# Performance work log

Measured on AMD Instinct MI355X. Metric: run time of the kernel, lower is better.

The kernel has to match this reference:

```python
import jax, jax.numpy as jnp
import numpy as np

VOCAB_SIZE = 13
EMBED_DIM = 50
HIDDEN_DIM = 50
BATCH = 2048
SEQ_LEN = 2048


def setup_inputs() -> dict:
    key = jax.random.key(0)
    ks = jax.random.split(key, 10)
    s = 0.1
    return {
        "x": jax.random.randint(ks[0], (BATCH, SEQ_LEN), 0, VOCAB_SIZE),
        "embed": jax.random.normal(ks[1], (VOCAB_SIZE, EMBED_DIM), jnp.float32),
        "W_ih": jax.random.normal(ks[2], (4 * HIDDEN_DIM, EMBED_DIM), jnp.float32) * s,
        "W_hh": jax.random.normal(ks[3], (4 * HIDDEN_DIM, HIDDEN_DIM), jnp.float32) * s,
        "b_ih": jax.random.normal(ks[4], (4 * HIDDEN_DIM,), jnp.float32) * s,
        "b_hh": jax.random.normal(ks[5], (4 * HIDDEN_DIM,), jnp.float32) * s,
        "W1": jax.random.normal(ks[6], (HIDDEN_DIM, HIDDEN_DIM), jnp.float32) * s,
        "b1": jax.random.normal(ks[7], (HIDDEN_DIM,), jnp.float32) * s,
        "W2": jax.random.normal(ks[8], (1, HIDDEN_DIM), jnp.float32) * s,
        "b2": jax.random.normal(ks[9], (1,), jnp.float32) * s,
    }


def reference(x, embed, W_ih, W_hh, b_ih, b_hh, W1, b1, W2, b2):
    B = x.shape[0]
    H = HIDDEN_DIM
    embeds = embed[x]                    # [B, T, E]
    xs = jnp.swapaxes(embeds, 0, 1)      # [T, B, E] for scan over time

    def step(carry, xt):
        hx, cx = carry
        gates = xt @ W_ih.T + b_ih + hx @ W_hh.T + b_hh   # [B, 4H]
        i = jax.nn.sigmoid(gates[:, 0 * H:1 * H])
        f = jax.nn.sigmoid(gates[:, 1 * H:2 * H])
        g = jnp.tanh(gates[:, 2 * H:3 * H])
        o = jax.nn.sigmoid(gates[:, 3 * H:4 * H])
        cx = f * cx + i * g
        hx = o * jnp.tanh(cx)
        return (hx, cx), None

    init = (jnp.zeros((B, H), embeds.dtype), jnp.zeros((B, H), embeds.dtype))
    (hx, _), _ = jax.lax.scan(step, init, xs)

    h = jax.nn.relu(hx @ W1.T + b1)
    out = (h @ W2.T + b2).squeeze(1)     # [B]
    return out
```

## Files before the change

### kernel.cpp

```cpp
#include <hip/hip_runtime.h>
#include <hip/hip_fp16.h>

#define T_SEQ 2048
#define HID   50
#define KP    64
#define MB    4
#define NBLK  512
#define NTHR  256
#define HSTR  80
#define BUFB  (MB*HSTR)

#define NLOG2E  1.4426950408889634f
#define N2LOG2E 2.8853900817779268f

typedef __attribute__((ext_vector_type(8))) _Float16 half8;
typedef __attribute__((ext_vector_type(4))) float    f32x4;

__device__ __forceinline__ ushort f16b(float f){ return __half_as_ushort(__float2half(f)); }
__device__ __forceinline__ float rcp_(float x){ return __builtin_amdgcn_rcpf(x); }
__device__ __forceinline__ float ex2_(float x){ return __builtin_amdgcn_exp2f(x); }

__global__ void build_B(const float* __restrict__ embed, const float* __restrict__ Wih,
                        const float* __restrict__ Whh, const float* __restrict__ bih,
                        const float* __restrict__ bhh, ushort* __restrict__ Bm) {
    int idx = blockIdx.x * blockDim.x + threadIdx.x;
    if (idx >= 256 * KP) return;
    int col = idx >> 6, k = idx & 63;
    int wq = col >> 6, g = (col >> 4) & 3, cc = col & 15;
    int u = wq * 16 + cc;
    ushort v = 0;
    if (u < HID) {
        int r = g * HID + u;
        float s = (g == 2) ? -N2LOG2E : -NLOG2E;
        if (k < HID) {
            v = f16b(s * Whh[r * HID + k]);
        } else if (k < 63) {
            float t = 0.f;
            for (int e = 0; e < HID; ++e)
                t = fmaf(embed[(k - 50) * HID + e], Wih[r * HID + e], t);
            v = f16b(s * t);
        } else {
            v = f16b(s * (bih[r] + bhh[r]));
        }
    }
    Bm[idx] = v;
}

__global__ __launch_bounds__(NTHR, 2) void lstm4(
    const int*    __restrict__ x,
    const ushort* __restrict__ Bm,
    const float*  __restrict__ W1,
    const float*  __restrict__ b1,
    const float*  __restrict__ W2,
    const float*  __restrict__ b2,
    float*        __restrict__ out)
{
    const int t   = threadIdx.x;
    const int w   = t >> 6;
    const int l   = t & 63;
    const int q   = l >> 4;
    const int c16 = l & 15;
    const int u   = w * 16 + c16;
    const int wu  = __builtin_amdgcn_readfirstlane(w);

    __shared__ __align__(16) ushort hbuf[2 * BUFB];
    __shared__ float zb[HID * MB];

    half8 bf[4][2];
    {
        const ushort* bp = Bm + (w * 64 + c16) * KP + q * 8;
        #pragma unroll
        for (int j = 0; j < 4; ++j) {
            bf[j][0] = *(const half8*)(bp + j * 16 * KP);
            bf[j][1] = *(const half8*)(bp + j * 16 * KP + 32);
        }
    }
    #pragma unroll
    for (int j = 0; j < 4; ++j)
        asm volatile("" : "+v"(bf[j][0]), "+v"(bf[j][1]));

    for (int i = t; i < 2 * BUFB; i += NTHR) hbuf[i] = 0;

    const int  row0 = blockIdx.x * MB;
    const int* xrow = x + (long)row0 * T_SEQ + (long)wu * T_SEQ;
    __syncthreads();
    int tk0 = xrow[0];
    int tk1 = xrow[1];
    if (l == 0) {
        hbuf[0 * BUFB + wu * HSTR + 63] = 0x3C00;
        hbuf[1 * BUFB + wu * HSTR + 63] = 0x3C00;
        hbuf[0 * BUFB + wu * HSTR + 50 + tk0] = 0x3C00;
        hbuf[1 * BUFB + wu * HSTR + 50 + tk1] = 0x3C00;
    }
    int t0r = tk1, t1r = tk0, t2r = tk1;
    __syncthreads();

    {
        uint slot = __builtin_amdgcn_s_getreg(6148) & 0xF;
        if (slot & 1) __builtin_amdgcn_s_sleep(6);
    }

    const ushort* ar  = hbuf + (c16 >> 2) * HSTR + q * 8;
    ushort*       wr_ = hbuf + q * HSTR + u;
    ushort*       hbw = hbuf + wu * HSTR + 50;

    float cs = 0.f;

#define STEP(P) do {                                                              \
        int it = step + 2 + (P); if (it > T_SEQ - 1) it = T_SEQ - 1;              \
        int tknf = xrow[it];                     \
        half8 a0 = *(const half8*)(ar + (P) * BUFB);                              \
        half8 a1 = *(const half8*)(ar + (P) * BUFB + 32);                         \
        const f32x4 zz = {0.f, 0.f, 0.f, 0.f};                                    \
        __builtin_amdgcn_s_setprio(1);                                            \
        f32x4 z0 = __builtin_amdgcn_mfma_f32_16x16x32_f16(a0, bf[0][0], zz,0,0,0);\
        z0 = __builtin_amdgcn_mfma_f32_16x16x32_f16(a1, bf[0][1], z0, 0,0,0);     \
        f32x4 z1 = __builtin_amdgcn_mfma_f32_16x16x32_f16(a0, bf[1][0], zz,0,0,0);\
        z1 = __builtin_amdgcn_mfma_f32_16x16x32_f16(a1, bf[1][1], z1, 0,0,0);     \
        f32x4 z2 = __builtin_amdgcn_mfma_f32_16x16x32_f16(a0, bf[2][0], zz,0,0,0);\
        z2 = __builtin_amdgcn_mfma_f32_16x16x32_f16(a1, bf[2][1], z2, 0,0,0);     \
        f32x4 z3 = __builtin_amdgcn_mfma_f32_16x16x32_f16(a0, bf[3][0], zz,0,0,0);\
        z3 = __builtin_amdgcn_mfma_f32_16x16x32_f16(a1, bf[3][1], z3, 0,0,0);     \
        __builtin_amdgcn_s_setprio(0);                                            \
           \
        float pi = ex2_(fminf(z0[0], 30.f));                          \
        float pf = ex2_(fminf(z1[0], 30.f));                          \
        float qg = ex2_(fminf(z2[0], 30.f));                          \
        float Df = 1.f + pf;                                                      \
        float D2 = (1.f + pi) * (1.f + qg);                                       \
        float iv1 = rcp_(Df * D2);                                                \
        float fv  = iv1 * D2;                                       \
        float igs = iv1 * Df * fmaf(N2LOG2E, qg, -N2LOG2E);      \
        cs = fmaf(fv, cs, igs);                                                   \
        float po = ex2_(fminf(z3[0], 30.f));                          \
        float qc = ex2_(fminf(cs, 30.f));                       \
        float iv2 = rcp_((1.f + po) * (1.f + qc));                                \
        float hh  = iv2 * (1.f - qc);                       \
        if (u < HID) wr_[(1 - (P)) * BUFB] = f16b(hh);                            \
        if (l == 0) {                                                             \
            ushort* hb = hbw + (1 - (P)) * BUFB;                                  \
            hb[t0r] = 0;                                                          \
            hb[t2r] = 0x3C00;                                                     \
        }                                                                         \
        t0r = t1r; t1r = t2r; t2r = tknf;                                         \
        __syncthreads();                                                          \
    } while (0)

    #pragma unroll 1
    for (int step = 0; step < T_SEQ; step += 2) {
        STEP(0);
        STEP(1);
    }
#undef STEP

    if (t < MB * HID) {
        int m = t & 3, uu = t >> 2;
        float a = b1[uu];
        const ushort* hr = hbuf + m * HSTR;
        #pragma unroll 10
        for (int k = 0; k < HID; ++k)
            a = fmaf(W1[uu * HID + k], __half2float(__ushort_as_half(hr[k])), a);
        zb[uu * MB + m] = fmaxf(a, 0.f);
    }
    __syncthreads();
    if (t < MB) {
        float a = b2[0];
        #pragma unroll 10
        for (int j = 0; j < HID; ++j)
            a = fmaf(W2[j], zb[j * MB + t], a);
        out[row0 + t] = a;
    }
}

extern "C" void kernel_launch(void* const* d_in, const int* in_sizes, int n_in,
                              void* d_out, int out_size, void* d_ws, size_t ws_size,
                              hipStream_t stream) {
    const int*   x     = (const int*)  d_in[0];
    const float* embed = (const float*)d_in[1];
    const float* W_ih  = (const float*)d_in[2];
    const float* W_hh  = (const float*)d_in[3];
    const float* b_ih  = (const float*)d_in[4];
    const float* b_hh  = (const float*)d_in[5];
    const float* W1    = (const float*)d_in[6];
    const float* b1    = (const float*)d_in[7];
    const float* W2    = (const float*)d_in[8];
    const float* b2    = (const float*)d_in[9];
    float* out = (float*)d_out;

    ushort* Bm = (ushort*)d_ws;

    build_B<<<(256 * KP + NTHR - 1) / NTHR, NTHR, 0, stream>>>(
        embed, W_ih, W_hh, b_ih, b_hh, Bm);

    lstm4<<<NBLK, NTHR, 0, stream>>>(
        x, Bm, W1, b1, W2, b2, out);
}
```

Before: 692.7 us.

## Interleave two independent batch groups per block and stage tokens in LDS

Each block now processes 8 sequences as two independent 4-row groups, issuing both groups' MFMAs and gate math within one step so the two dependency chains can hide each other's latency under a single barrier. The grid is halved to 256 blocks with launch bounds of 1 block per CU. Token indices for the block are preloaded into LDS as bytes, replacing per-step global loads. The per-slot sleep and setprio tricks are removed. In exchange, per-step instruction count doubles and occupancy drops, which can lengthen the serial step if latency was not the bottleneck.

After: 954.0 us. 1.38x slower.

```diff
diff --git a/kernel.cpp b/kernel.cpp
--- a/kernel.cpp
+++ b/kernel.cpp
@@ -4,11 +4,11 @@
 #define T_SEQ 2048
 #define HID   50
 #define KP    64
-#define MB    4
-#define NBLK  512
+#define MBG   4
+#define NBLK  256
 #define NTHR  256
 #define HSTR  80
-#define BUFB  (MB*HSTR)
+#define BUFB  (MBG*HSTR)
 
 #define NLOG2E  1.4426950408889634f
 #define N2LOG2E 2.8853900817779268f
@@ -46,7 +46,7 @@
     Bm[idx] = v;
 }
 
-__global__ __launch_bounds__(NTHR, 2) void lstm4(
+__global__ __launch_bounds__(NTHR, 1) void lstm_dual(
     const int*    __restrict__ x,
     const ushort* __restrict__ Bm,
     const float*  __restrict__ W1,
@@ -61,10 +61,11 @@
     const int q   = l >> 4;
     const int c16 = l & 15;
     const int u   = w * 16 + c16;
-    const int wu  = __builtin_amdgcn_readfirstlane(w);
-
-    __shared__ __align__(16) ushort hbuf[2 * BUFB];
-    __shared__ float zb[HID * MB];
+
+    __shared__ __align__(16) ushort hb0[2 * BUFB];
+    __shared__ __align__(16) ushort hb1[2 * BUFB];
+    __shared__ __align__(16) unsigned char tokL[8 * T_SEQ];
+    __shared__ float zb[HID * 8];
 
     half8 bf[4][2];
     {
@@ -79,70 +80,104 @@
     for (int j = 0; j < 4; ++j)
         asm volatile("" : "+v"(bf[j][0]), "+v"(bf[j][1]));
 
-    for (int i = t; i < 2 * BUFB; i += NTHR) hbuf[i] = 0;
-
-    const int  row0 = blockIdx.x * MB;
-    const int* xrow = x + (long)row0 * T_SEQ + (long)wu * T_SEQ;
+    {
+        const int4* xs = (const int4*)(x + (long)blockIdx.x * 8 * T_SEQ);
+        for (int i = t; i < 8 * T_SEQ / 4; i += NTHR) {
+            int4 v = xs[i];
+            uint pk = (uint)(v.x & 0xFF) | ((uint)(v.y & 0xFF) << 8) |
+                      ((uint)(v.z & 0xFF) << 16) | ((uint)(v.w & 0xFF) << 24);
+            *(uint*)(tokL + i * 4) = pk;
+        }
+    }
+    for (int i = t; i < 2 * BUFB; i += NTHR) { hb0[i] = 0; hb1[i] = 0; }
     __syncthreads();
-    int tk0 = xrow[0];
-    int tk1 = xrow[1];
-    if (l == 0) {
-        hbuf[0 * BUFB + wu * HSTR + 63] = 0x3C00;
-        hbuf[1 * BUFB + wu * HSTR + 63] = 0x3C00;
-        hbuf[0 * BUFB + wu * HSTR + 50 + tk0] = 0x3C00;
-        hbuf[1 * BUFB + wu * HSTR + 50 + tk1] = 0x3C00;
-    }
-    int t0r = tk1, t1r = tk0, t2r = tk1;
+
+    int tA0, tA1, tA2, tB0, tB1, tB2;
+    {
+        int k00 = tokL[w * T_SEQ + 0],       k01 = tokL[w * T_SEQ + 1];
+        int k10 = tokL[(4 + w) * T_SEQ + 0], k11 = tokL[(4 + w) * T_SEQ + 1];
+        if (l == 0) {
+            hb0[0 * BUFB + w * HSTR + 63] = 0x3C00;
+            hb0[1 * BUFB + w * HSTR + 63] = 0x3C00;
+            hb0[0 * BUFB + w * HSTR + 50 + k00] = 0x3C00;
+            hb0[1 * BUFB + w * HSTR + 50 + k01] = 0x3C00;
+            hb1[0 * BUFB + w * HSTR + 63] = 0x3C00;
+            hb1[1 * BUFB + w * HSTR + 63] = 0x3C00;
+            hb1[0 * BUFB + w * HSTR + 50 + k10] = 0x3C00;
+            hb1[1 * BUFB + w * HSTR + 50 + k11] = 0x3C00;
+        }
+        tA0 = k01; tA1 = k00; tA2 = k01;
+        tB0 = k11; tB1 = k10; tB2 = k11;
+    }
     __syncthreads();
 
-    {
-        uint slot = __builtin_amdgcn_s_getreg(6148) & 0xF;
-        if (slot & 1) __builtin_amdgcn_s_sleep(6);
-    }
-
-    const ushort* ar  = hbuf + (c16 >> 2) * HSTR + q * 8;
-    ushort*       wr_ = hbuf + q * HSTR + u;
-    ushort*       hbw = hbuf + wu * HSTR + 50;
-
-    float cs = 0.f;
-
+    const ushort* ar0 = hb0 + (c16 >> 2) * HSTR + q * 8;
+    const ushort* ar1 = hb1 + (c16 >> 2) * HSTR + q * 8;
+    ushort*       wr0 = hb0 + q * HSTR + u;
+    ushort*       wr1 = hb1 + q * HSTR + u;
+    const unsigned char* tp0 = tokL + w * T_SEQ;
+    const unsigned char* tp1 = tokL + (4 + w) * T_SEQ;
+
+    float cs0 = 0.f, cs1 = 0.f;
+
+#define MFMA_(A,B,C) __builtin_amdgcn_mfma_f32_16x16x32_f16((A),(B),(C),0,0,0)
 #define STEP(P) do {                                                              \
         int it = step + 2 + (P); if (it > T_SEQ - 1) it = T_SEQ - 1;              \
-        int tknf = xrow[it];                     \
-        half8 a0 = *(const half8*)(ar + (P) * BUFB);                              \
-        half8 a1 = *(const half8*)(ar + (P) * BUFB + 32);                         \
+        int tn0 = tp0[it];                               \
+        int tn1 = tp1[it];                                                        \
+        half8 a00 = *(const half8*)(ar0 + (P) * BUFB);                            \
+        half8 a01 = *(const half8*)(ar0 + (P) * BUFB + 32);                       \
+        half8 a10 = *(const half8*)(ar1 + (P) * BUFB);                            \
+        half8 a11 = *(const half8*)(ar1 + (P) * BUFB + 32);                       \
         const f32x4 zz = {0.f, 0.f, 0.f, 0.f};                                    \
-        __builtin_amdgcn_s_setprio(1);                                            \
-        f32x4 z0 = __builtin_amdgcn_mfma_f32_16x16x32_f16(a0, bf[0][0], zz,0,0,0);\
-        z0 = __builtin_amdgcn_mfma_f32_16x16x32_f16(a1, bf[0][1], z0, 0,0,0);     \
-        f32x4 z1 = __builtin_amdgcn_mfma_f32_16x16x32_f16(a0, bf[1][0], zz,0,0,0);\
-        z1 = __builtin_amdgcn_mfma_f32_16x16x32_f16(a1, bf[1][1], z1, 0,0,0);     \
-        f32x4 z2 = __builtin_amdgcn_mfma_f32_16x16x32_f16(a0, bf[2][0], zz,0,0,0);\
-        z2 = __builtin_amdgcn_mfma_f32_16x16x32_f16(a1, bf[2][1], z2, 0,0,0);     \
-        f32x4 z3 = __builtin_amdgcn_mfma_f32_16x16x32_f16(a0, bf[3][0], zz,0,0,0);\
-        z3 = __builtin_amdgcn_mfma_f32_16x16x32_f16(a1, bf[3][1], z3, 0,0,0);     \
-        __builtin_amdgcn_s_setprio(0);                                            \
-           \
-        float pi = ex2_(fminf(z0[0], 30.f));                          \
-        float pf = ex2_(fminf(z1[0], 30.f));                          \
-        float qg = ex2_(fminf(z2[0], 30.f));                          \
-        float Df = 1.f + pf;                                                      \
-        float D2 = (1.f + pi) * (1.f + qg);                                       \
-        float iv1 = rcp_(Df * D2);                                                \
-        float fv  = iv1 * D2;                                       \
-        float igs = iv1 * Df * fmaf(N2LOG2E, qg, -N2LOG2E);      \
-        cs = fmaf(fv, cs, igs);                                                   \
-        float po = ex2_(fminf(z3[0], 30.f));                          \
-        float qc = ex2_(fminf(cs, 30.f));                       \
-        float iv2 = rcp_((1.f + po) * (1.f + qc));                                \
-        float hh  = iv2 * (1.f - qc);                       \
-        if (u < HID) wr_[(1 - (P)) * BUFB] = f16b(hh);                            \
+        f32x4 z0 = MFMA_(a00, bf[0][0], zz); z0 = MFMA_(a01, bf[0][1], z0);       \
+        f32x4 z1 = MFMA_(a00, bf[1][0], zz); z1 = MFMA_(a01, bf[1][1], z1);       \
+        f32x4 z2 = MFMA_(a00, bf[2][0], zz); z2 = MFMA_(a01, bf[2][1], z2);       \
+        f32x4 z3 = MFMA_(a00, bf[3][0], zz); z3 = MFMA_(a01, bf[3][1], z3);       \
+        f32x4 y0 = MFMA_(a10, bf[0][0], zz); y0 = MFMA_(a11, bf[0][1], y0);       \
+        f32x4 y1 = MFMA_(a10, bf[1][0], zz); y1 = MFMA_(a11, bf[1][1], y1);       \
+        f32x4 y2 = MFMA_(a10, bf[2][0], zz); y2 = MFMA_(a11, bf[2][1], y2);       \
+        f32x4 y3 = MFMA_(a10, bf[3][0], zz); y3 = MFMA_(a11, bf[3][1], y3);       \
+          \
+        float pi0 = ex2_(fminf(z0[0], 30.f));                                     \
+        float pf0 = ex2_(fminf(z1[0], 30.f));                                     \
+        float qg0 = ex2_(fminf(z2[0], 30.f));                                     \
+        float Df0 = 1.f + pf0;                                                    \
+        float D20 = (1.f + pi0) * (1.f + qg0);                                    \
+        float ivA = rcp_(Df0 * D20);                                              \
+        float fv0 = ivA * D20;                                                    \
+        float ig0 = ivA * Df0 * fmaf(N2LOG2E, qg0, -N2LOG2E);                     \
+        cs0 = fmaf(fv0, cs0, ig0);                                                \
+        float po0 = ex2_(fminf(z3[0], 30.f));                                     \
+        float qc0 = ex2_(fminf(cs0, 30.f));                                       \
+        float ivB = rcp_((1.f + po0) * (1.f + qc0));                              \
+        float h0  = ivB * (1.f - qc0);                                            \
+                   \
+        float pi1 = ex2_(fminf(y0[0], 30.f));                                     \
+        float pf1 = ex2_(fminf(y1[0], 30.f));                                     \
+        float qg1 = ex2_(fminf(y2[0], 30.f));                                     \
+        float Df1 = 1.f + pf1;                                                    \
+        float D21 = (1.f + pi1) * (1.f + qg1);                                    \
+        float ivC = rcp_(Df1 * D21);                                              \
+        float fv1 = ivC * D21;                                                    \
+        float ig1 = ivC * Df1 * fmaf(N2LOG2E, qg1, -N2LOG2E);                     \
+        cs1 = fmaf(fv1, cs1, ig1);                                                \
+        float po1 = ex2_(fminf(y3[0], 30.f));                                     \
+        float qc1 = ex2_(fminf(cs1, 30.f));                                       \
+        float ivD = rcp_((1.f + po1) * (1.f + qc1));                              \
+        float h1  = ivD * (1.f - qc1);                                            \
+        if (u < HID) {                                                            \
+            wr0[(1 - (P)) * BUFB] = f16b(h0);                                     \
+            wr1[(1 - (P)) * BUFB] = f16b(h1);                                     \
+        }                                                                         \
         if (l == 0) {                                                             \
-            ushort* hb = hbw + (1 - (P)) * BUFB;                                  \
-            hb[t0r] = 0;                                                          \
-            hb[t2r] = 0x3C00;                                                     \
+            ushort* p0 = hb0 + (1 - (P)) * BUFB + w * HSTR + 50;                  \
+            p0[tA0] = 0;  p0[tA2] = 0x3C00;                                       \
+            ushort* p1 = hb1 + (1 - (P)) * BUFB + w * HSTR + 50;                  \
+            p1[tB0] = 0;  p1[tB2] = 0x3C00;                                       \
         }                                                                         \
-        t0r = t1r; t1r = t2r; t2r = tknf;                                         \
+        tA0 = tA1; tA1 = tA2; tA2 = tn0;                                          \
+        tB0 = tB1; tB1 = tB2; tB2 = tn1;                                          \
         __syncthreads();                                                          \
     } while (0)
 
@@ -152,23 +187,24 @@
         STEP(1);
     }
 #undef STEP
-
-    if (t < MB * HID) {
-        int m = t & 3, uu = t >> 2;
+#undef MFMA_
+
+    for (int idx = t; idx < 8 * HID; idx += NTHR) {
+        int m = idx & 7, uu = idx >> 3;
+        const ushort* hr = (m < 4 ? hb0 : hb1) + (m & 3) * HSTR;
         float a = b1[uu];
-        const ushort* hr = hbuf + m * HSTR;
         #pragma unroll 10
         for (int k = 0; k < HID; ++k)
             a = fmaf(W1[uu * HID + k], __half2float(__ushort_as_half(hr[k])), a);
-        zb[uu * MB + m] = fmaxf(a, 0.f);
+        zb[uu * 8 + m] = fmaxf(a, 0.f);
     }
     __syncthreads();
-    if (t < MB) {
+    if (t < 8) {
         float a = b2[0];
         #pragma unroll 10
         for (int j = 0; j < HID; ++j)
-            a = fmaf(W2[j], zb[j * MB + t], a);
-        out[row0 + t] = a;
+            a = fmaf(W2[j], zb[j * 8 + t], a);
+        out[blockIdx.x * 8 + t] = a;
     }
 }
 
@@ -192,6 +228,6 @@
     build_B<<<(256 * KP + NTHR - 1) / NTHR, NTHR, 0, stream>>>(
         embed, W_ih, W_hh, b_ih, b_hh, Bm);
 
-    lstm4<<<NBLK, NTHR, 0, stream>>>(
+    lstm_dual<<<NBLK, NTHR, 0, stream>>>(
         x, Bm, W1, b1, W2, b2, out);
 }
```

## Use 8 waves per block handling 8 rows, with DPP gate exchange and LDS tokens

Applied to the files above, without the earlier changes.

Blocks now hold 8 sequences across 8 waves (256 blocks of 512 threads). Each wave covers 8 hidden units using half the MFMAs per step, and the gate columns held in each lane's other half are swapped in with a DPP row-swap. All tokens for the block are preloaded into LDS as bytes, which takes per-step global loads off the serial recurrence path, and the wave-slot sleep staggering is removed. The cost is a 512-thread barrier every step and only 256 blocks, which may leave CUs underused or make synchronisation heavier.

Result: slower. 748.3 us (+8.0%).

```diff
diff --git a/kernel.cpp b/kernel.cpp
--- a/kernel.cpp
+++ b/kernel.cpp
@@ -4,9 +4,9 @@
 #define T_SEQ 2048
 #define HID   50
 #define KP    64
-#define MB    4
-#define NBLK  512
-#define NTHR  256
+#define MB    8
+#define NBLK  256
+#define NTHR  512
 #define HSTR  80
 #define BUFB  (MB*HSTR)
 
@@ -19,6 +19,9 @@
 __device__ __forceinline__ ushort f16b(float f){ return __half_as_ushort(__float2half(f)); }
 __device__ __forceinline__ float rcp_(float x){ return __builtin_amdgcn_rcpf(x); }
 __device__ __forceinline__ float ex2_(float x){ return __builtin_amdgcn_exp2f(x); }
+__device__ __forceinline__ float dpp_swap8(float v){
+    return __int_as_float(__builtin_amdgcn_mov_dpp(__float_as_int(v), 0x128, 0xF, 0xF, true));
+}
 
 __global__ void build_B(const float* __restrict__ embed, const float* __restrict__ Wih,
                         const float* __restrict__ Whh, const float* __restrict__ bih,
@@ -26,8 +29,9 @@
     int idx = blockIdx.x * blockDim.x + threadIdx.x;
     if (idx >= 256 * KP) return;
     int col = idx >> 6, k = idx & 63;
-    int wq = col >> 6, g = (col >> 4) & 3, cc = col & 15;
-    int u = wq * 16 + cc;
+    int w = col >> 5, j = (col >> 4) & 1, cc = col & 15;
+    int g = 2 * j + (cc >> 3);
+    int u = 8 * w + (cc & 7);
     ushort v = 0;
     if (u < HID) {
         int r = g * HID + u;
@@ -46,7 +50,7 @@
     Bm[idx] = v;
 }
 
-__global__ __launch_bounds__(NTHR, 2) void lstm4(
+__global__ __launch_bounds__(NTHR, 2) void lstm8w(
     const int*    __restrict__ x,
     const ushort* __restrict__ Bm,
     const float*  __restrict__ W1,
@@ -55,94 +59,103 @@
     const float*  __restrict__ b2,
     float*        __restrict__ out)
 {
-    const int t   = threadIdx.x;
-    const int w   = t >> 6;
-    const int l   = t & 63;
-    const int q   = l >> 4;
-    const int c16 = l & 15;
-    const int u   = w * 16 + c16;
-    const int wu  = __builtin_amdgcn_readfirstlane(w);
+    const int t    = threadIdx.x;
+    const int w    = t >> 6;
+    const int l    = t & 63;
+    const int q    = l >> 4;
+    const int c16  = l & 15;
+    const bool lo  = (c16 < 8);
+    const int u    = 8 * w + (c16 & 7);
+    const int myrow = 2 * q + (lo ? 0 : 1);
 
     __shared__ __align__(16) ushort hbuf[2 * BUFB];
+    __shared__ __align__(16) unsigned char tokL[MB * T_SEQ];
     __shared__ float zb[HID * MB];
 
-    half8 bf[4][2];
+    half8 bf[2][2];
     {
-        const ushort* bp = Bm + (w * 64 + c16) * KP + q * 8;
+        const ushort* bp = Bm + (w * 32 + c16) * KP + q * 8;
         #pragma unroll
-        for (int j = 0; j < 4; ++j) {
+        for (int j = 0; j < 2; ++j) {
             bf[j][0] = *(const half8*)(bp + j * 16 * KP);
             bf[j][1] = *(const half8*)(bp + j * 16 * KP + 32);
         }
     }
-    #pragma unroll
-    for (int j = 0; j < 4; ++j)
-        asm volatile("" : "+v"(bf[j][0]), "+v"(bf[j][1]));
-
+    asm volatile("" : "+v"(bf[0][0]), "+v"(bf[0][1]), "+v"(bf[1][0]), "+v"(bf[1][1]));
+
+    {
+        const int4* xs = (const int4*)(x + (long)blockIdx.x * MB * T_SEQ);
+        for (int i = t; i < MB * T_SEQ / 4; i += NTHR) {
+            int4 v = xs[i];
+            uint pk = (uint)(v.x & 0xFF) | ((uint)(v.y & 0xFF) << 8) |
+                      ((uint)(v.z & 0xFF) << 16) | ((uint)(v.w & 0xFF) << 24);
+            *(uint*)(tokL + i * 4) = pk;
+        }
+    }
     for (int i = t; i < 2 * BUFB; i += NTHR) hbuf[i] = 0;
-
-    const int  row0 = blockIdx.x * MB;
-    const int* xrow = x + (long)row0 * T_SEQ + (long)wu * T_SEQ;
     __syncthreads();
-    int tk0 = xrow[0];
-    int tk1 = xrow[1];
+
+    int tk0 = tokL[w * T_SEQ + 0];
+    int tk1 = tokL[w * T_SEQ + 1];
     if (l == 0) {
-        hbuf[0 * BUFB + wu * HSTR + 63] = 0x3C00;
-        hbuf[1 * BUFB + wu * HSTR + 63] = 0x3C00;
-        hbuf[0 * BUFB + wu * HSTR + 50 + tk0] = 0x3C00;
-        hbuf[1 * BUFB + wu * HSTR + 50 + tk1] = 0x3C00;
+        hbuf[0 * BUFB + w * HSTR + 63] = 0x3C00;
+        hbuf[1 * BUFB + w * HSTR + 63] = 0x3C00;
+        hbuf[0 * BUFB + w * HSTR + 50 + tk0] = 0x3C00;
+        hbuf[1 * BUFB + w * HSTR + 50 + tk1] = 0x3C00;
     }
     int t0r = tk1, t1r = tk0, t2r = tk1;
     __syncthreads();
 
-    {
-        uint slot = __builtin_amdgcn_s_getreg(6148) & 0xF;
-        if (slot & 1) __builtin_amdgcn_s_sleep(6);
-    }
-
-    const ushort* ar  = hbuf + (c16 >> 2) * HSTR + q * 8;
-    ushort*       wr_ = hbuf + q * HSTR + u;
-    ushort*       hbw = hbuf + wu * HSTR + 50;
+    const ushort* ar  = hbuf + (c16 >> 1) * HSTR + q * 8;
+    ushort*       wr_ = hbuf + myrow * HSTR + u;
+    const unsigned char* tp = tokL + w * T_SEQ;
 
     float cs = 0.f;
 
+#define MFMA_(A,B,C) __builtin_amdgcn_mfma_f32_16x16x32_f16((A),(B),(C),0,0,0)
 #define STEP(P) do {                                                              \
         int it = step + 2 + (P); if (it > T_SEQ - 1) it = T_SEQ - 1;              \
-        int tknf = xrow[it];                     \
+        int tn = tp[it];                                  \
         half8 a0 = *(const half8*)(ar + (P) * BUFB);                              \
         half8 a1 = *(const half8*)(ar + (P) * BUFB + 32);                         \
         const f32x4 zz = {0.f, 0.f, 0.f, 0.f};                                    \
         __builtin_amdgcn_s_setprio(1);                                            \
-        f32x4 z0 = __builtin_amdgcn_mfma_f32_16x16x32_f16(a0, bf[0][0], zz,0,0,0);\
-        z0 = __builtin_amdgcn_mfma_f32_16x16x32_f16(a1, bf[0][1], z0, 0,0,0);     \
-        f32x4 z1 = __builtin_amdgcn_mfma_f32_16x16x32_f16(a0, bf[1][0], zz,0,0,0);\
-        z1 = __builtin_amdgcn_mfma_f32_16x16x32_f16(a1, bf[1][1], z1, 0,0,0);     \
-        f32x4 z2 = __builtin_amdgcn_mfma_f32_16x16x32_f16(a0, bf[2][0], zz,0,0,0);\
-        z2 = __builtin_amdgcn_mfma_f32_16x16x32_f16(a1, bf[2][1], z2, 0,0,0);     \
-        f32x4 z3 = __builtin_amdgcn_mfma_f32_16x16x32_f16(a0, bf[3][0], zz,0,0,0);\
-        z3 = __builtin_amdgcn_mfma_f32_16x16x32_f16(a1, bf[3][1], z3, 0,0,0);     \
+        f32x4 z0a = MFMA_(a0, bf[0][0], zz);    \
+        f32x4 z0b = MFMA_(a1, bf[0][1], zz);                                      \
+        f32x4 z1a = MFMA_(a0, bf[1][0], zz);                                      \
+        f32x4 z1b = MFMA_(a1, bf[1][1], zz);                                      \
         __builtin_amdgcn_s_setprio(0);                                            \
-           \
-        float pi = ex2_(fminf(z0[0], 30.f));                          \
-        float pf = ex2_(fminf(z1[0], 30.f));                          \
-        float qg = ex2_(fminf(z2[0], 30.f));                          \
+        float s0l = z0a[0] + z0b[0];                     \
+        float s0h = z0a[2] + z0b[2];                     \
+        float s1l = z1a[0] + z1b[0];                     \
+        float s1h = z1a[2] + z1b[2];                     \
+        float rx0 = dpp_swap8(lo ? s0h : s0l);    \
+        float rx1 = dpp_swap8(lo ? s1h : s1l);                                    \
+        float gi = lo ? s0l : rx0;                  \
+        float gf = lo ? rx0 : s0h;                                                \
+        float gg = lo ? s1l : rx1;                                                \
+        float go = lo ? rx1 : s1h;                                                \
+                        \
+        float pi = ex2_(fminf(gi, 30.f));                                         \
+        float pf = ex2_(fminf(gf, 30.f));                                         \
+        float qg = ex2_(fminf(gg, 30.f));                                         \
         float Df = 1.f + pf;                                                      \
         float D2 = (1.f + pi) * (1.f + qg);                                       \
-        float iv1 = rcp_(Df * D2);                                                \
-        float fv  = iv1 * D2;                                       \
-        float igs = iv1 * Df * fmaf(N2LOG2E, qg, -N2LOG2E);      \
+        float ivA = rcp_(Df * D2);                                                \
+        float fv  = ivA * D2;                                       \
+        float igs = ivA * Df * fmaf(N2LOG2E, qg, -N2LOG2E);      \
         cs = fmaf(fv, cs, igs);                                                   \
-        float po = ex2_(fminf(z3[0], 30.f));                          \
+        float po = ex2_(fminf(go, 30.f));                                         \
         float qc = ex2_(fminf(cs, 30.f));                       \
-        float iv2 = rcp_((1.f + po) * (1.f + qc));                                \
-        float hh  = iv2 * (1.f - qc);                       \
+        float ivB = rcp_((1.f + po) * (1.f + qc));                                \
+        float hh  = ivB * (1.f - qc);                       \
         if (u < HID) wr_[(1 - (P)) * BUFB] = f16b(hh);                            \
         if (l == 0) {                                                             \
-            ushort* hb = hbw + (1 - (P)) * BUFB;                                  \
+            ushort* hb = hbuf + (1 - (P)) * BUFB + w * HSTR + 50;                 \
             hb[t0r] = 0;                                                          \
             hb[t2r] = 0x3C00;                                                     \
         }                                                                         \
-        t0r = t1r; t1r = t2r; t2r = tknf;                                         \
+        t0r = t1r; t1r = t2r; t2r = tn;                                           \
         __syncthreads();                                                          \
     } while (0)
 
@@ -152,9 +165,10 @@
         STEP(1);
     }
 #undef STEP
+#undef MFMA_
 
     if (t < MB * HID) {
-        int m = t & 3, uu = t >> 2;
+        int m = t & 7, uu = t >> 3;
         float a = b1[uu];
         const ushort* hr = hbuf + m * HSTR;
         #pragma unroll 10
@@ -168,7 +182,7 @@
         #pragma unroll 10
         for (int j = 0; j < HID; ++j)
             a = fmaf(W2[j], zb[j * MB + t], a);
-        out[row0 + t] = a;
+        out[blockIdx.x * MB + t] = a;
     }
 }
 
@@ -189,9 +203,9 @@
 
     ushort* Bm = (ushort*)d_ws;
 
-    build_B<<<(256 * KP + NTHR - 1) / NTHR, NTHR, 0, stream>>>(
+    build_B<<<(256 * KP + 255) / 256, 256, 0, stream>>>(
         embed, W_ih, W_hh, b_ih, b_hh, Bm);
 
-    lstm4<<<NBLK, NTHR, 0, stream>>>(
+    lstm8w<<<NBLK, NTHR, 0, stream>>>(
         x, Bm, W1, b1, W2, b2, out);
 }
```
